# Kernel optimization log

Hardware: AMD Instinct MI355X
Metric: run time of the kernel (lower is better)

## Reference

```python
import jax, jax.numpy as jnp
import numpy as np

EPS = 1e-7
T_NCE = 0.07      # opt.nce_t
MOMENTUM = 0.5    # opt.nce_m
N_DATA = 100000   # opt.n_data


def l2norm(x):
    # Normalize(power=2): x / (sum(x^2, dim=1))^(1/2)
    return x / jnp.sqrt(jnp.sum(x * x, axis=1, keepdims=True))


def contrast_loss(x, P):
    # ContrastLoss (Eq 18). x: [B, P+K] of normalized exp-similarities.
    B, PK = x.shape
    N = PK - P
    m_pn = N * (1.0 / N_DATA)  # m * Pn
    pos = x[:, :P]                                   # [B, P]
    log_D1 = jnp.log(pos / (pos + m_pn + EPS))
    neg = x[:, P:]                                   # [B, N]
    log_D0 = jnp.log(m_pn / (neg + m_pn + EPS))
    # log_D0.view(-1,1).repeat(1,P).sum(0) == P copies of log_D0.sum()
    return -((log_D1.sum(0) + log_D0.sum()) / B).sum() / P


def setup_inputs() -> dict:
    key = jax.random.key(0)
    ks = jax.random.split(key, 10)
    B, S_DIM, T_DIM, FEAT = 64, 2048, 2048, 128
    P, K = 4, 8192
    NCLS, PER = 7, 1000
    stdv = 1.0 / np.sqrt(FEAT / 3.0)
    return {
        "f_s": jax.random.normal(ks[0], (B, S_DIM), jnp.float32),
        "f_t": jax.random.normal(ks[1], (B, T_DIM), jnp.float32),
        "idx": jax.random.randint(ks[2], (B,), 0, N_DATA),
        "batch_label": jax.random.uniform(ks[3], (B, NCLS), dtype=jnp.float32),
        "class_index": jax.random.randint(ks[4], (NCLS, PER), 0, N_DATA),
        "num_pos": P,
        "contrast_idx": jax.random.randint(ks[5], (B, P + K), 0, N_DATA),
        "W_s": jax.random.normal(ks[6], (S_DIM, FEAT), jnp.float32) * 0.02,
        "b_s": jnp.zeros((FEAT,), jnp.float32),
        "W_t": jax.random.normal(ks[7], (T_DIM, FEAT), jnp.float32) * 0.02,
        "b_t": jnp.zeros((FEAT,), jnp.float32),
        "memory_s": jax.random.uniform(ks[8], (N_DATA, FEAT), jnp.float32, -stdv, stdv),
        "memory_t": jax.random.uniform(ks[9], (N_DATA, FEAT), jnp.float32, -stdv, stdv),
    }


def reference(f_s, f_t, idx, batch_label, class_index, num_pos, contrast_idx,
              W_s, b_s, W_t, b_t, memory_s, memory_t):
    # Embed + L2 norm
    f_s = l2norm(f_s @ W_s + b_s)   # [B, D]
    f_t = l2norm(f_t @ W_t + b_t)   # [B, D]

    # ContrastMemory (memory banks are buffers -> no grad through them)
    mem_s = jax.lax.stop_gradient(memory_s)
    mem_t = jax.lax.stop_gradient(memory_t)

    w_t = mem_t[contrast_idx]                                     # [B, P+K, D]
    out_s = jnp.exp(jnp.einsum('bkd,bd->bk', w_t, f_s) / T_NCE)
    out_s = out_s / (jnp.mean(out_s) * N_DATA)                    # Z_s normalization
    w_s = mem_s[contrast_idx]                                     # [B, P+K, D]
    out_t = jnp.exp(jnp.einsum('bkd,bd->bk', w_s, f_t) / T_NCE)
    out_t = out_t / (jnp.mean(out_t) * N_DATA)                    # Z_t normalization

    # momentum memory update (done under no_grad in torch)
    upd_s = l2norm(mem_s[idx] * MOMENTUM + jax.lax.stop_gradient(f_s) * (1.0 - MOMENTUM))
    new_mem_s = mem_s.at[idx].set(upd_s)
    upd_t = l2norm(mem_t[idx] * MOMENTUM + jax.lax.stop_gradient(f_t) * (1.0 - MOMENTUM))
    new_mem_t = mem_t.at[idx].set(upd_t)

    CCD_loss = contrast_loss(out_s, num_pos) + contrast_loss(out_t, num_pos)

    # class-center anchors: gather per-class memory rows, relu, mean -> [NCLS, D]
    s_anchors = l2norm(jnp.mean(jax.nn.relu(new_mem_s[class_index]), axis=1))
    t_anchors = l2norm(jnp.mean(jax.nn.relu(new_mem_t[class_index]), axis=1))

    # anchor relation loss (anchors detached; teacher relation fully detached)
    s_rel = (f_s @ jax.lax.stop_gradient(s_anchors).T) / T_NCE    # [B, NCLS]
    t_rel = jax.lax.stop_gradient((f_t @ t_anchors.T) / T_NCE)
    targets = jax.nn.softmax(t_rel, axis=1)
    log_inputs = jax.nn.log_softmax(s_rel, axis=1)
    relation_loss = jnp.sum(targets * (jnp.log(targets + EPS * 0 + 1e-30) - log_inputs)) / s_rel.shape[0]

    return (CCD_loss, relation_loss, f_s, f_t)
```

## Files before the change

kernel.cpp:

```cpp
#include <hip/hip_runtime.h>
#include <math.h>
#include <stdint.h>

#define B 64
#define SDIM 2048
#define FEAT 128
#define P 4
#define PK 8196
#define NCLS 7
#define PER 1000
#define NDATA 100000
#define EPSC 1e-7f
#define M_PN 0.08192f
#define JCHUNKS 50
#define CS (PER / JCHUNKS)

#define DTSZ (64 * NDATA)
#define KSPLIT 4
#define KSEG 2049
#define KS1 8
#define TPW 4
#define ROWS_BLK (4 * TPW * 16)

#define TILE 16
#define WCHUNK 512
#define NT (WCHUNK / TILE)

#define GLL16(gp, lp) \
    __builtin_amdgcn_global_load_lds( \
        (__attribute__((address_space(1))) void*)(uintptr_t)(gp), \
        (__attribute__((address_space(3))) void*)(lp), 16, 0, 0)

typedef __attribute__((ext_vector_type(8))) short bf16x8;
typedef __attribute__((ext_vector_type(4))) float f32x4;

static __device__ __forceinline__ short f2bf(float x)
{
    union { float f; uint32_t u; } v; v.f = x;
    const uint32_t r = (v.u + 0x7fffu + ((v.u >> 16) & 1u)) >> 16;
    return (short)r;
}

__global__ void gemm_partial_kernel(const float* __restrict__ f_s,
                                    const float* __restrict__ f_t,
                                    const float* __restrict__ W_s,
                                    const float* __restrict__ W_t,
                                    float* __restrict__ fb)
{
    const int row = blockIdx.x;
    const int z   = blockIdx.y;
    const int ks  = blockIdx.z;
    const float* f = z == 0 ? f_s : f_t;
    const float* W = z == 0 ? W_s : W_t;

    const int t  = threadIdx.x;
    const int d  = t & 127;
    const int kh = t >> 7;

    __shared__ float frow[SDIM / KS1];
    frow[t] = f[row * SDIM + ks * (SDIM / KS1) + t];
    __syncthreads();

    float acc = 0.0f;
    const int kb = ks * (SDIM / KS1) + kh * 128;
    #pragma unroll 8
    for (int k = 0; k < 128; ++k)
        acc = fmaf(frow[kh * 128 + k], W[(kb + k) * FEAT + d], acc);

    __shared__ float part[2][128];
    part[kh][d] = acc;
    __syncthreads();
    if (t < 128)
        atomicAdd(&fb[((size_t)z * B + row) * FEAT + t], part[0][t] + part[1][t]);
}

__global__ void norm_finish_kernel(const float* __restrict__ fb,
                                   const float* __restrict__ b_s,
                                   const float* __restrict__ b_t,
                                   float* __restrict__ out_fs,
                                   float* __restrict__ out_ft,
                                   float* __restrict__ fsw,
                                   float* __restrict__ ftw,
                                   unsigned short* __restrict__ fsb,
                                   unsigned short* __restrict__ ftb)
{
    const int row = blockIdx.x;
    const int z   = blockIdx.y;
    const int d   = threadIdx.x;
    const float* bias = z == 0 ? b_s : b_t;
    float* out = z == 0 ? out_fs : out_ft;
    float* fw  = z == 0 ? fsw : ftw;
    unsigned short* fbx = z == 0 ? fsb : ftb;

    const float a = fb[((size_t)z * B + row) * FEAT + d] + bias[d];
    __shared__ float red[128];
    red[d] = a * a;
    __syncthreads();
    for (int s = 64; s > 0; s >>= 1) {
        if (d < s) red[d] += red[d + s];
        __syncthreads();
    }
    const float v = a * (1.0f / sqrtf(red[0]));
    out[row * FEAT + d] = v;
    fw[row * FEAT + d]  = v;
    fbx[row * FEAT + d] = (unsigned short)f2bf(v);
}

#define MFMA4(av, kc, a0, a1, a2, a3) do { \
    a0 = __builtin_amdgcn_mfma_f32_16x16x32_bf16(av, bv[kc][0], a0, 0, 0, 0); \
    a1 = __builtin_amdgcn_mfma_f32_16x16x32_bf16(av, bv[kc][1], a1, 0, 0, 0); \
    a2 = __builtin_amdgcn_mfma_f32_16x16x32_bf16(av, bv[kc][2], a2, 0, 0, 0); \
    a3 = __builtin_amdgcn_mfma_f32_16x16x32_bf16(av, bv[kc][3], a3, 0, 0, 0); \
    } while (0)

__global__ __launch_bounds__(256, 2)
void dgemm4_kernel(const unsigned short* __restrict__ fsb,
                   const unsigned short* __restrict__ ftb,
                   const float* __restrict__ mem_s,
                   const float* __restrict__ mem_t,
                   float* __restrict__ DT0,
                   float* __restrict__ DT1,
                   int zbase)
{
    const int z = blockIdx.y + zbase;
    const unsigned short* fWb = z == 0 ? fsb : ftb;
    const float* mem          = z == 0 ? mem_t : mem_s;
    float* DT                 = z == 0 ? DT0 : DT1;

    const int tid = threadIdx.x;
    const int w   = tid >> 6;
    const int l   = tid & 63;
    const int ln  = l & 15;
    const int ko  = l >> 4;
    const int xk  = ln & 7;
    const int wrowbase = blockIdx.x * ROWS_BLK + w * (TPW * 16);

    __shared__ __align__(16) float rows[4][2][16 * FEAT];

    bf16x8 bv[4][4];
    #pragma unroll
    for (int kc = 0; kc < 4; ++kc)
        #pragma unroll
        for (int nt = 0; nt < 4; ++nt)
            bv[kc][nt] = *(const bf16x8*)(fWb + (nt * 16 + ln) * FEAT + kc * 32 + ko * 8);

#define STG(tt, bf) do { \
    _Pragma("unroll") \
    for (int p_ = 0; p_ < 8; ++p_) { \
        const int r_ = 2 * p_ + (l >> 5); \
        int gr_ = wrowbase + (tt) * 16 + r_; \
        if (gr_ >= NDATA) gr_ = NDATA - 1; \
        const float* g_ = mem + (size_t)gr_ * FEAT + (((l & 31) ^ (r_ & 7)) << 2); \
        GLL16(g_, &rows[w][bf][p_ * 256]); \
    } } while (0)

    STG(0, 0);
    int cur = 0;
    for (int t = 0; t < TPW; ++t) {
        if (t + 1 < TPW) {
            STG(t + 1, cur ^ 1);
            asm volatile("s_waitcnt vmcnt(8)" ::: "memory");
        } else {
            asm volatile("s_waitcnt vmcnt(0)" ::: "memory");
        }
        __builtin_amdgcn_sched_barrier(0);

        const float* rb = &rows[w][cur][ln * FEAT];
        f32x4 c0 = (f32x4){0.f,0.f,0.f,0.f};
        f32x4 c1 = (f32x4){0.f,0.f,0.f,0.f};
        f32x4 c2 = (f32x4){0.f,0.f,0.f,0.f};
        f32x4 c3 = (f32x4){0.f,0.f,0.f,0.f};
        #pragma unroll
        for (int kc = 0; kc < 4; ++kc) {
            const int g0 = kc * 8 + ko * 2;
            const float4 lo = *(const float4*)(rb + (((g0 + 0) ^ xk) << 2));
            const float4 hi = *(const float4*)(rb + (((g0 + 1) ^ xk) << 2));
            const bf16x8 av = (bf16x8){ f2bf(lo.x), f2bf(lo.y), f2bf(lo.z), f2bf(lo.w),
                                        f2bf(hi.x), f2bf(hi.y), f2bf(hi.z), f2bf(hi.w) };
            MFMA4(av, kc, c0, c1, c2, c3);
        }

        const int growb = wrowbase + t * 16 + ko * 4;
        if (growb < NDATA) {
            *(f32x4*)(DT + (size_t)( 0 + ln) * NDATA + growb) = c0;
            *(f32x4*)(DT + (size_t)(16 + ln) * NDATA + growb) = c1;
            *(f32x4*)(DT + (size_t)(32 + ln) * NDATA + growb) = c2;
            *(f32x4*)(DT + (size_t)(48 + ln) * NDATA + growb) = c3;
        }
        cur ^= 1;
    }
#undef STG
}

__global__ void gather2_kernel(const int* __restrict__ contrast_idx,
                               const float* __restrict__ DT0,
                               const float* __restrict__ DT1,
                               float* __restrict__ out_raw,
                               float* __restrict__ Ssum)
{
    const int z   = blockIdx.z;
    const int b   = blockIdx.y;
    const int ks  = blockIdx.x;
    const int tid = threadIdx.x;
    const int k0  = ks * KSEG;
    const int kend = min(k0 + KSEG, PK);
    const float inv_t = 1.0f / 0.07f;
    const float* dtb = (z == 0 ? DT0 : DT1) + (size_t)b * NDATA;
    float* orz = out_raw + (size_t)z * (B * PK);
    float lsum = 0.0f;
    #pragma unroll 4
    for (int k = k0 + tid; k < kend; k += 256) {
        const int ci = contrast_idx[(size_t)b * PK + k];
        const float v = expf(dtb[ci] * inv_t);
        orz[(size_t)b * PK + k] = v;
        lsum += v;
    }
    __shared__ float red[256];
    red[tid] = lsum;
    __syncthreads();
    for (int s = 128; s > 0; s >>= 1) {
        if (tid < s) red[tid] += red[tid + s];
        __syncthreads();
    }
    if (tid == 0) atomicAdd(&Ssum[z], red[0]);
}

__global__ void gemm_norm_kernel(const float* __restrict__ f_s,
                                 const float* __restrict__ f_t,
                                 const float* __restrict__ W_s,
                                 const float* __restrict__ b_s,
                                 const float* __restrict__ W_t,
                                 const float* __restrict__ b_t,
                                 float* __restrict__ out_fs,
                                 float* __restrict__ out_ft)
{
    const int row = blockIdx.x;
    const int z   = blockIdx.y;
    const float* f    = z == 0 ? f_s : f_t;
    const float* W    = z == 0 ? W_s : W_t;
    const float* bias = z == 0 ? b_s : b_t;
    float* out        = z == 0 ? out_fs : out_ft;

    __shared__ __align__(16) float frow[SDIM];
    const int t  = threadIdx.x;
    const int d  = t & 127;
    const int kh = t >> 7;
    for (int k = t; k < SDIM; k += 256) frow[k] = f[row * SDIM + k];
    __syncthreads();

    float acc = 0.0f;
    const int k0 = kh * (SDIM / 2);
    for (int k = k0; k < k0 + SDIM / 2; ++k)
        acc = fmaf(frow[k], W[k * FEAT + d], acc);

    __shared__ float part[2][128];
    part[kh][d] = acc;
    __syncthreads();
    const float a = part[0][d] + part[1][d] + bias[d];

    __shared__ float red[256];
    red[t] = (t < 128) ? a * a : 0.0f;
    __syncthreads();
    for (int s = 128; s > 0; s >>= 1) {
        if (t < s) red[t] += red[t + s];
        __syncthreads();
    }
    if (t < 128) out[row * FEAT + t] = a * (1.0f / sqrtf(red[0]));
}

__global__ __launch_bounds__(64)
void dots_kernel(const float* __restrict__ fsn,
                 const float* __restrict__ ftn,
                 const int*   __restrict__ contrast_idx,
                 const float* __restrict__ mem_s,
                 const float* __restrict__ mem_t,
                 float* __restrict__ out_raw,
                 float* __restrict__ Ssum)
{
    const int z = blockIdx.z;
    const int b = blockIdx.y;
    const int l = threadIdx.x;
    const int kchunk = blockIdx.x * WCHUNK;

    const float* f   = (z == 0 ? fsn : ftn) + b * FEAT;
    const float* mem = (z == 0 ? mem_t : mem_s);

    __shared__ __align__(16) float rows[2][TILE * FEAT];
    __shared__ __align__(16) float fl[FEAT];
    __shared__ int cis[WCHUNK];

    fl[l]      = f[l];
    fl[l + 64] = f[l + 64];
    for (int i = l; i < WCHUNK; i += 64) {
        const int k = kchunk + i;
        cis[i] = contrast_idx[(size_t)b * PK + (k < PK ? k : PK - 1)];
    }
    __syncthreads();

    const int q   = l >> 4;
    const int r_c = l & 15;
    const int xk  = r_c & 7;
    const int rh  = l >> 5;
    const int sl  = l & 31;

    const float4* fg = (const float4*)fl;
    const float4 f0 = fg[q * 8 + 0], f1 = fg[q * 8 + 1];
    const float4 f2 = fg[q * 8 + 2], f3 = fg[q * 8 + 3];
    const float4 f4 = fg[q * 8 + 4], f5 = fg[q * 8 + 5];
    const float4 f6 = fg[q * 8 + 6], f7 = fg[q * 8 + 7];

    const float inv_t = 1.0f / 0.07f;
    const size_t obase = (size_t)z * (B * PK) + (size_t)b * PK;
    float lsum = 0.0f;

#define STAGE(tt, bf) do { \
    _Pragma("unroll") \
    for (int p_ = 0; p_ < 8; ++p_) { \
        const int rr_ = 2 * p_ + rh; \
        const int ci_ = cis[(tt) * TILE + rr_]; \
        const float* g_ = mem + (size_t)ci_ * FEAT + ((sl ^ (rr_ & 7)) << 2); \
        GLL16(g_, &rows[bf][p_ * 256]); \
    } } while (0)

    STAGE(0, 0);
    int cur = 0;
    for (int t = 0; t < NT; ++t) {
        if (t + 1 < NT) {
            STAGE(t + 1, cur ^ 1);
            asm volatile("s_waitcnt vmcnt(8)" ::: "memory");
        } else {
            asm volatile("s_waitcnt vmcnt(0)" ::: "memory");
        }
        __builtin_amdgcn_sched_barrier(0);

        const float* rbase = &rows[cur][r_c * FEAT];
        float dot;
        {
            const float4 m0 = *(const float4*)(rbase + (((q * 8 + 0) ^ xk) << 2));
            const float4 m1 = *(const float4*)(rbase + (((q * 8 + 1) ^ xk) << 2));
            const float4 m2 = *(const float4*)(rbase + (((q * 8 + 2) ^ xk) << 2));
            const float4 m3 = *(const float4*)(rbase + (((q * 8 + 3) ^ xk) << 2));
            const float4 m4 = *(const float4*)(rbase + (((q * 8 + 4) ^ xk) << 2));
            const float4 m5 = *(const float4*)(rbase + (((q * 8 + 5) ^ xk) << 2));
            const float4 m6 = *(const float4*)(rbase + (((q * 8 + 6) ^ xk) << 2));
            const float4 m7 = *(const float4*)(rbase + (((q * 8 + 7) ^ xk) << 2));
            dot = m0.x * f0.x;
            dot = fmaf(m0.y, f0.y, dot); dot = fmaf(m0.z, f0.z, dot); dot = fmaf(m0.w, f0.w, dot);
            dot = fmaf(m1.x, f1.x, dot); dot = fmaf(m1.y, f1.y, dot); dot = fmaf(m1.z, f1.z, dot); dot = fmaf(m1.w, f1.w, dot);
            dot = fmaf(m2.x, f2.x, dot); dot = fmaf(m2.y, f2.y, dot); dot = fmaf(m2.z, f2.z, dot); dot = fmaf(m2.w, f2.w, dot);
            dot = fmaf(m3.x, f3.x, dot); dot = fmaf(m3.y, f3.y, dot); dot = fmaf(m3.z, f3.z, dot); dot = fmaf(m3.w, f3.w, dot);
            dot = fmaf(m4.x, f4.x, dot); dot = fmaf(m4.y, f4.y, dot); dot = fmaf(m4.z, f4.z, dot); dot = fmaf(m4.w, f4.w, dot);
            dot = fmaf(m5.x, f5.x, dot); dot = fmaf(m5.y, f5.y, dot); dot = fmaf(m5.z, f5.z, dot); dot = fmaf(m5.w, f5.w, dot);
            dot = fmaf(m6.x, f6.x, dot); dot = fmaf(m6.y, f6.y, dot); dot = fmaf(m6.z, f6.z, dot); dot = fmaf(m6.w, f6.w, dot);
            dot = fmaf(m7.x, f7.x, dot); dot = fmaf(m7.y, f7.y, dot); dot = fmaf(m7.z, f7.z, dot); dot = fmaf(m7.w, f7.w, dot);
        }
        dot += __shfl_xor(dot, 16);
        dot += __shfl_xor(dot, 32);

        const int krow = kchunk + t * TILE + r_c;
        if (q == 0 && krow < PK) {
            const float val = expf(dot * inv_t);
            out_raw[obase + krow] = val;
            lsum += val;
        }
        cur ^= 1;
    }
#undef STAGE

    lsum += __shfl_xor(lsum, 8);
    lsum += __shfl_xor(lsum, 4);
    lsum += __shfl_xor(lsum, 2);
    lsum += __shfl_xor(lsum, 1);
    if (l == 0) atomicAdd(&Ssum[z], lsum);
}

__global__ void ccd_loss_kernel(const float* __restrict__ out_raw,
                                const float* __restrict__ Ssum,
                                float* __restrict__ acc)
{
    const int z = blockIdx.y;
    const float S = Ssum[z];
    const float c = ((float)(B * PK)) / (S * (float)NDATA);

    const int total = B * PK;
    float contrib = 0.0f;
    for (int i = blockIdx.x * blockDim.x + threadIdx.x; i < total;
         i += gridDim.x * blockDim.x) {
        const float v = out_raw[(size_t)z * total + i] * c;
        const int k = i % PK;
        if (k < P) {
            contrib += logf(v / (v + M_PN + EPSC));
        } else {
            contrib += (float)P * logf(M_PN / (v + M_PN + EPSC));
        }
    }
    __shared__ float red[256];
    red[threadIdx.x] = contrib;
    __syncthreads();
    for (int s = 128; s > 0; s >>= 1) {
        if (threadIdx.x < s) red[threadIdx.x] += red[threadIdx.x + s];
        __syncthreads();
    }
    if (threadIdx.x == 0) atomicAdd(&acc[z], red[0]);
}

__global__ void upd_kernel(const float* __restrict__ fsn,
                           const float* __restrict__ ftn,
                           const int*   __restrict__ idx,
                           const float* __restrict__ mem_s,
                           const float* __restrict__ mem_t,
                           float* __restrict__ upd)
{
    const int z = blockIdx.y;
    const int b = blockIdx.x;
    const int d = threadIdx.x;
    const float* mem = z == 0 ? mem_s : mem_t;
    const float* f   = z == 0 ? fsn : ftn;
    const int i = idx[b];
    const float v = mem[(size_t)i * FEAT + d] * 0.5f + f[b * FEAT + d] * 0.5f;
    __shared__ float red[128];
    red[d] = v * v;
    __syncthreads();
    for (int s = 64; s > 0; s >>= 1) {
        if (d < s) red[d] += red[d + s];
        __syncthreads();
    }
    upd[(size_t)z * (B * FEAT) + b * FEAT + d] = v * (1.0f / sqrtf(red[0]));
}

__global__ void remap_kernel(const int* __restrict__ class_index,
                             const int* __restrict__ idx,
                             int* __restrict__ remap)
{
    const int e = blockIdx.x * 256 + threadIdx.x;
    if (e >= NCLS * PER) return;
    const int ci = class_index[e];
    int rb = -1;
    for (int b = B - 1; b >= 0; --b) {
        if (idx[b] == ci) { rb = b; break; }
    }
    remap[e] = rb;
}

__global__ void anchors_partial_kernel(const int* __restrict__ class_index,
                                       const int* __restrict__ remap,
                                       const float* __restrict__ mem_s,
                                       const float* __restrict__ mem_t,
                                       const float* __restrict__ upd,
                                       float* __restrict__ partial)
{
    const int z     = blockIdx.z;
    const int c     = blockIdx.y;
    const int chunk = blockIdx.x;
    const int d     = threadIdx.x;
    const float* mem = z == 0 ? mem_s : mem_t;
    const float* u   = upd + (size_t)z * (B * FEAT);
    float acc = 0.0f;
    #pragma unroll 4
    for (int j = chunk * CS; j < chunk * CS + CS; ++j) {
        const int e = c * PER + j;
        const int ci = class_index[e];
        const int rb = remap[e];
        const float* row = (rb >= 0) ? (u + rb * FEAT) : (mem + (size_t)ci * FEAT);
        const float v = row[d];
        acc += v > 0.0f ? v : 0.0f;
    }
    atomicAdd(&partial[(size_t)z * (NCLS * FEAT) + c * FEAT + d], acc);
}

__global__ void anchors_finish_kernel(const float* __restrict__ partial,
                                      float* __restrict__ anchors)
{
    const int z = blockIdx.y;
    const int c = blockIdx.x;
    const int d = threadIdx.x;
    const float meanv = partial[(size_t)z * (NCLS * FEAT) + c * FEAT + d]
                        * (1.0f / (float)PER);
    __shared__ float red[128];
    red[d] = meanv * meanv;
    __syncthreads();
    for (int s = 64; s > 0; s >>= 1) {
        if (d < s) red[d] += red[d + s];
        __syncthreads();
    }
    anchors[(size_t)z * (NCLS * FEAT) + c * FEAT + d] = meanv * (1.0f / sqrtf(red[0]));
}

__global__ void final_kernel(const float* __restrict__ fsn,
                             const float* __restrict__ ftn,
                             const float* __restrict__ anchors,
                             const float* __restrict__ acc,
                             float* __restrict__ d_out)
{
    __shared__ float sa[NCLS * FEAT];
    __shared__ float ta[NCLS * FEAT];
    const int tid = threadIdx.x;
    for (int i = tid; i < NCLS * FEAT; i += 64) {
        sa[i] = anchors[i];
        ta[i] = anchors[NCLS * FEAT + i];
    }
    __syncthreads();

    const int b = tid;
    float srel[NCLS], trel[NCLS];
    for (int j = 0; j < NCLS; ++j) { srel[j] = 0.0f; trel[j] = 0.0f; }
    for (int d = 0; d < FEAT; ++d) {
        const float fs = fsn[b * FEAT + d];
        const float ft = ftn[b * FEAT + d];
        #pragma unroll
        for (int j = 0; j < NCLS; ++j) {
            srel[j] = fmaf(fs, sa[j * FEAT + d], srel[j]);
            trel[j] = fmaf(ft, ta[j * FEAT + d], trel[j]);
        }
    }
    const float inv_t = 1.0f / 0.07f;
    float smax = -1e30f, tmax = -1e30f;
    for (int j = 0; j < NCLS; ++j) {
        srel[j] *= inv_t; trel[j] *= inv_t;
        smax = fmaxf(smax, srel[j]);
        tmax = fmaxf(tmax, trel[j]);
    }
    float ssum = 0.0f, tsum = 0.0f;
    float texp[NCLS];
    for (int j = 0; j < NCLS; ++j) {
        ssum += expf(srel[j] - smax);
        texp[j] = expf(trel[j] - tmax);
        tsum += texp[j];
    }
    const float lse_s = logf(ssum);
    float contrib = 0.0f;
    for (int j = 0; j < NCLS; ++j) {
        const float tgt = texp[j] / tsum;
        const float log_in = srel[j] - smax - lse_s;
        contrib += tgt * (logf(tgt + 1e-30f) - log_in);
    }
    for (int off = 32; off > 0; off >>= 1) contrib += __shfl_down(contrib, off);
    if (tid == 0) {
        d_out[1] = contrib / (float)B;
        d_out[0] = -(acc[0] + acc[1]) / (float)(B * P);
    }
}

extern "C" void kernel_launch(void* const* d_in, const int* in_sizes, int n_in,
                              void* d_out_v, int out_size, void* d_ws, size_t ws_size,
                              hipStream_t stream)
{
    const float* f_s = (const float*)d_in[0];
    const float* f_t = (const float*)d_in[1];
    const int*   idx = (const int*)d_in[2];
    const int*   class_index = (const int*)d_in[4];
    const int*   contrast_idx = (const int*)d_in[6];
    const float* W_s = (const float*)d_in[7];
    const float* b_s = (const float*)d_in[8];
    const float* W_t = (const float*)d_in[9];
    const float* b_t = (const float*)d_in[10];
    const float* mem_s = (const float*)d_in[11];
    const float* mem_t = (const float*)d_in[12];

    float* out    = (float*)d_out_v;
    float* out_fs = out + 2;
    float* out_ft = out + 2 + B * FEAT;

    float* ws = (float*)d_ws;
    const size_t fl = ws_size / sizeof(float);
    const size_t REST = 2 * (size_t)B * PK
                      + 2 * B * FEAT
                      + 2 * (B * FEAT / 2)
                      + 2 * B * FEAT
                      + 2 * B * FEAT
                      + 4 * NCLS * FEAT
                      + NCLS * PER
                      + 64;
    const bool big   = fl >= 2 * (size_t)DTSZ + REST;
    const bool small = fl >= 1 * (size_t)DTSZ + REST;

    if (small) {
        float* DT0 = ws;
        float* DT1 = big ? ws + DTSZ : DT0;
        float* p   = (big ? ws + 2 * (size_t)DTSZ : ws + DTSZ);
        float* out_raw = p;            p += 2 * (size_t)B * PK;
        float* fsw     = p;            p += B * FEAT;
        float* ftw     = p;            p += B * FEAT;
        unsigned short* fsb = (unsigned short*)p;  p += B * FEAT / 2;
        unsigned short* ftb = (unsigned short*)p;  p += B * FEAT / 2;
        float* fb      = p;            p += 2 * B * FEAT;
        float* partial = p;            p += 2 * NCLS * FEAT;
        float* Ssum    = p;            p += 2;
        float* acc     = p;            p += 2;
        float* upd     = p;            p += 2 * B * FEAT;
        float* anchors = p;            p += 2 * NCLS * FEAT;
        int*   remap   = (int*)p;

        hipMemsetAsync(fb, 0,
                       (2 * B * FEAT + 2 * NCLS * FEAT + 4) * sizeof(float),
                       stream);

        dim3 g1a(B, 2, KS1);
        gemm_partial_kernel<<<g1a, 256, 0, stream>>>(f_s, f_t, W_s, W_t, fb);
        dim3 g1b(B, 2);
        norm_finish_kernel<<<g1b, 128, 0, stream>>>(fb, b_s, b_t,
                                                    out_fs, out_ft,
                                                    fsw, ftw, fsb, ftb);

        const int gblocks = (NDATA + ROWS_BLK - 1) / ROWS_BLK;
        if (big) {
            dim3 gd(gblocks, 2);
            dgemm4_kernel<<<gd, 256, 0, stream>>>(fsb, ftb, mem_s, mem_t,
                                                  DT0, DT1, 0);
            dim3 gg(KSPLIT, B, 2);
            gather2_kernel<<<gg, 256, 0, stream>>>(contrast_idx, DT0, DT1,
                                                   out_raw, Ssum);
        } else {
            dim3 gd(gblocks, 1);
            dim3 gg(KSPLIT, B, 1);
            dgemm4_kernel<<<gd, 256, 0, stream>>>(fsb, ftb, mem_s, mem_t,
                                                  DT0, DT0, 0);
            gather2_kernel<<<gg, 256, 0, stream>>>(contrast_idx, DT0, DT0,
                                                   out_raw, Ssum);
            dgemm4_kernel<<<gd, 256, 0, stream>>>(fsb, ftb, mem_s, mem_t,
                                                  DT0, DT0, 1);
            gather2_kernel<<<gg, 256, 0, stream>>>(contrast_idx, DT0, DT0,
                                                   out_raw + (size_t)B * PK,
                                                   Ssum + 1);
        }

        dim3 g3(256, 2);
        ccd_loss_kernel<<<g3, 256, 0, stream>>>(out_raw, Ssum, acc);
        dim3 g4(B, 2);
        upd_kernel<<<g4, 128, 0, stream>>>(out_fs, out_ft, idx, mem_s, mem_t, upd);
        remap_kernel<<<(NCLS * PER + 255) / 256, 256, 0, stream>>>(class_index, idx, remap);
        dim3 g5a(JCHUNKS, NCLS, 2);
        anchors_partial_kernel<<<g5a, 128, 0, stream>>>(class_index, remap,
                                                        mem_s, mem_t, upd, partial);
        dim3 g5b(NCLS, 2);
        anchors_finish_kernel<<<g5b, 128, 0, stream>>>(partial, anchors);
        final_kernel<<<1, 64, 0, stream>>>(out_fs, out_ft, anchors, acc, out);
    } else {
        float* out_raw = ws;
        float* upd     = out_raw + 2 * (B * PK);
        float* anchors = upd + 2 * (B * FEAT);
        float* partial = anchors + 2 * (NCLS * FEAT);
        float* Ssum    = partial + 2 * (NCLS * FEAT);
        float* acc     = Ssum + 2;
        int*   remap   = (int*)(acc + 2);

        hipMemsetAsync(partial, 0, (2 * NCLS * FEAT + 4) * sizeof(float), stream);

        dim3 g1(B, 2);
        gemm_norm_kernel<<<g1, 256, 0, stream>>>(f_s, f_t, W_s, b_s, W_t, b_t,
                                                 out_fs, out_ft);
        dim3 g2((PK + WCHUNK - 1) / WCHUNK, B, 2);
        dots_kernel<<<g2, 64, 0, stream>>>(out_fs, out_ft, contrast_idx,
                                           mem_s, mem_t, out_raw, Ssum);
        dim3 g3(256, 2);
        ccd_loss_kernel<<<g3, 256, 0, stream>>>(out_raw, Ssum, acc);
        dim3 g4(B, 2);
        upd_kernel<<<g4, 128, 0, stream>>>(out_fs, out_ft, idx, mem_s, mem_t, upd);
        remap_kernel<<<(NCLS * PER + 255) / 256, 256, 0, stream>>>(class_index, idx, remap);
        dim3 g5a(JCHUNKS, NCLS, 2);
        anchors_partial_kernel<<<g5a, 128, 0, stream>>>(class_index, remap,
                                                        mem_s, mem_t, upd, partial);
        dim3 g5b(NCLS, 2);
        anchors_finish_kernel<<<g5b, 128, 0, stream>>>(partial, anchors);
        final_kernel<<<1, 64, 0, stream>>>(out_fs, out_ft, anchors, acc, out);
    }
}
```

Baseline: 118.6 us.

## Recompute gathered similarities in a fused loss pass and shrink dgemm blocks

The gather kernel no longer writes the exponentiated similarities to a buffer. Instead it only accumulates the normalisation sum, and a second pass re-gathers from the dot-product table to compute the contrastive loss terms directly, which removes the separate ccd_loss kernel and the large out_raw round trip. The redundant fp32 copies of the normalised features are also dropped. The bf16 GEMM over the memory bank now uses 2 waves per block instead of 4, giving more, smaller blocks. The price is a second round of random gathers and exp evaluations over the dot-product table.

```diff
diff --git a/kernel.cpp b/kernel.cpp
--- a/kernel.cpp
+++ b/kernel.cpp
@@ -20,7 +20,8 @@
 #define KSEG 2049
 #define KS1 8
 #define TPW 4
-#define ROWS_BLK (4 * TPW * 16)
+#define WVS 2
+#define ROWS_BLK (WVS * TPW * 16)
 
 #define TILE 16
 #define WCHUNK 512
@@ -79,8 +80,6 @@
                                    const float* __restrict__ b_t,
                                    float* __restrict__ out_fs,
                                    float* __restrict__ out_ft,
-                                   float* __restrict__ fsw,
-                                   float* __restrict__ ftw,
                                    unsigned short* __restrict__ fsb,
                                    unsigned short* __restrict__ ftb)
 {
@@ -89,7 +88,6 @@
     const int d   = threadIdx.x;
     const float* bias = z == 0 ? b_s : b_t;
     float* out = z == 0 ? out_fs : out_ft;
-    float* fw  = z == 0 ? fsw : ftw;
     unsigned short* fbx = z == 0 ? fsb : ftb;
 
     const float a = fb[((size_t)z * B + row) * FEAT + d] + bias[d];
@@ -102,7 +100,6 @@
     }
     const float v = a * (1.0f / sqrtf(red[0]));
     out[row * FEAT + d] = v;
-    fw[row * FEAT + d]  = v;
     fbx[row * FEAT + d] = (unsigned short)f2bf(v);
 }
 
@@ -113,8 +110,8 @@
     a3 = __builtin_amdgcn_mfma_f32_16x16x32_bf16(av, bv[kc][3], a3, 0, 0, 0); \
     } while (0)
 
-__global__ __launch_bounds__(256, 2)
-void dgemm4_kernel(const unsigned short* __restrict__ fsb,
+__global__ __launch_bounds__(WVS * 64, 2)
+void dgemm5_kernel(const unsigned short* __restrict__ fsb,
                    const unsigned short* __restrict__ ftb,
                    const float* __restrict__ mem_s,
                    const float* __restrict__ mem_t,
@@ -135,7 +132,7 @@
     const int xk  = ln & 7;
     const int wrowbase = blockIdx.x * ROWS_BLK + w * (TPW * 16);
 
-    __shared__ __align__(16) float rows[4][2][16 * FEAT];
+    __shared__ __align__(16) float rows[WVS][2][16 * FEAT];
 
     bf16x8 bv[4][4];
     #pragma unroll
@@ -192,11 +189,10 @@
 #undef STG
 }
 
-__global__ void gather2_kernel(const int* __restrict__ contrast_idx,
-                               const float* __restrict__ DT0,
-                               const float* __restrict__ DT1,
-                               float* __restrict__ out_raw,
-                               float* __restrict__ Ssum)
+__global__ void gather_s_kernel(const int* __restrict__ contrast_idx,
+                                const float* __restrict__ DT0,
+                                const float* __restrict__ DT1,
+                                float* __restrict__ Ssum)
 {
     const int z   = blockIdx.z;
     const int b   = blockIdx.y;
@@ -206,14 +202,11 @@
     const int kend = min(k0 + KSEG, PK);
     const float inv_t = 1.0f / 0.07f;
     const float* dtb = (z == 0 ? DT0 : DT1) + (size_t)b * NDATA;
-    float* orz = out_raw + (size_t)z * (B * PK);
     float lsum = 0.0f;
     #pragma unroll 4
     for (int k = k0 + tid; k < kend; k += 256) {
         const int ci = contrast_idx[(size_t)b * PK + k];
-        const float v = expf(dtb[ci] * inv_t);
-        orz[(size_t)b * PK + k] = v;
-        lsum += v;
+        lsum += expf(dtb[ci] * inv_t);
     }
     __shared__ float red[256];
     red[tid] = lsum;
@@ -223,6 +216,40 @@
         __syncthreads();
     }
     if (tid == 0) atomicAdd(&Ssum[z], red[0]);
+}
+
+__global__ void loss2_kernel(const int* __restrict__ contrast_idx,
+                             const float* __restrict__ DT0,
+                             const float* __restrict__ DT1,
+                             const float* __restrict__ Ssum,
+                             float* __restrict__ acc)
+{
+    const int z   = blockIdx.z;
+    const int b   = blockIdx.y;
+    const int ks  = blockIdx.x;
+    const int tid = threadIdx.x;
+    const int k0  = ks * KSEG;
+    const int kend = min(k0 + KSEG, PK);
+    const float inv_t = 1.0f / 0.07f;
+    const float S = Ssum[z];
+    const float c = ((float)(B * PK)) / (S * (float)NDATA);
+    const float* dtb = (z == 0 ? DT0 : DT1) + (size_t)b * NDATA;
+    float contrib = 0.0f;
+    #pragma unroll 4
+    for (int k = k0 + tid; k < kend; k += 256) {
+        const int ci = contrast_idx[(size_t)b * PK + k];
+        const float v = expf(dtb[ci] * inv_t) * c;
+        if (k < P) contrib += logf(v / (v + M_PN + EPSC));
+        else       contrib += (float)P * logf(M_PN / (v + M_PN + EPSC));
+    }
+    __shared__ float red[256];
+    red[tid] = contrib;
+    __syncthreads();
+    for (int s = 128; s > 0; s >>= 1) {
+        if (tid < s) red[tid] += red[tid + s];
+        __syncthreads();
+    }
+    if (tid == 0) atomicAdd(&acc[z], red[0]);
 }
 
 __global__ void gemm_norm_kernel(const float* __restrict__ f_s,
@@ -563,9 +590,7 @@
 
     float* ws = (float*)d_ws;
     const size_t fl = ws_size / sizeof(float);
-    const size_t REST = 2 * (size_t)B * PK
-                      + 2 * B * FEAT
-                      + 2 * (B * FEAT / 2)
+    const size_t REST = (size_t)B * FEAT
                       + 2 * B * FEAT
                       + 2 * B * FEAT
                       + 4 * NCLS * FEAT
@@ -573,14 +598,12 @@
                       + 64;
     const bool big   = fl >= 2 * (size_t)DTSZ + REST;
     const bool small = fl >= 1 * (size_t)DTSZ + REST;
+    const size_t RESTFB = 2 * (size_t)B * PK + REST;
 
     if (small) {
         float* DT0 = ws;
         float* DT1 = big ? ws + DTSZ : DT0;
         float* p   = (big ? ws + 2 * (size_t)DTSZ : ws + DTSZ);
-        float* out_raw = p;            p += 2 * (size_t)B * PK;
-        float* fsw     = p;            p += B * FEAT;
-        float* ftw     = p;            p += B * FEAT;
         unsigned short* fsb = (unsigned short*)p;  p += B * FEAT / 2;
         unsigned short* ftb = (unsigned short*)p;  p += B * FEAT / 2;
         float* fb      = p;            p += 2 * B * FEAT;
@@ -599,33 +622,30 @@
         gemm_partial_kernel<<<g1a, 256, 0, stream>>>(f_s, f_t, W_s, W_t, fb);
         dim3 g1b(B, 2);
         norm_finish_kernel<<<g1b, 128, 0, stream>>>(fb, b_s, b_t,
-                                                    out_fs, out_ft,
-                                                    fsw, ftw, fsb, ftb);
+                                                    out_fs, out_ft, fsb, ftb);
 
         const int gblocks = (NDATA + ROWS_BLK - 1) / ROWS_BLK;
         if (big) {
             dim3 gd(gblocks, 2);
-            dgemm4_kernel<<<gd, 256, 0, stream>>>(fsb, ftb, mem_s, mem_t,
-                                                  DT0, DT1, 0);
+            dgemm5_kernel<<<gd, WVS * 64, 0, stream>>>(fsb, ftb, mem_s, mem_t,
+                                                       DT0, DT1, 0);
             dim3 gg(KSPLIT, B, 2);
-            gather2_kernel<<<gg, 256, 0, stream>>>(contrast_idx, DT0, DT1,
-                                                   out_raw, Ssum);
+            gather_s_kernel<<<gg, 256, 0, stream>>>(contrast_idx, DT0, DT1, Ssum);
+            loss2_kernel<<<gg, 256, 0, stream>>>(contrast_idx, DT0, DT1, Ssum, acc);
         } else {
             dim3 gd(gblocks, 1);
             dim3 gg(KSPLIT, B, 1);
-            dgemm4_kernel<<<gd, 256, 0, stream>>>(fsb, ftb, mem_s, mem_t,
-                                                  DT0, DT0, 0);
-            gather2_kernel<<<gg, 256, 0, stream>>>(contrast_idx, DT0, DT0,
-                                                   out_raw, Ssum);
-            dgemm4_kernel<<<gd, 256, 0, stream>>>(fsb, ftb, mem_s, mem_t,
-                                                  DT0, DT0, 1);
-            gather2_kernel<<<gg, 256, 0, stream>>>(contrast_idx, DT0, DT0,
-                                                   out_raw + (size_t)B * PK,
-                                                   Ssum + 1);
-        }
-
-        dim3 g3(256, 2);
-        ccd_loss_kernel<<<g3, 256, 0, stream>>>(out_raw, Ssum, acc);
+            dgemm5_kernel<<<gd, WVS * 64, 0, stream>>>(fsb, ftb, mem_s, mem_t,
+                                                       DT0, DT0, 0);
+            gather_s_kernel<<<gg, 256, 0, stream>>>(contrast_idx, DT0, DT0, Ssum);
+            loss2_kernel<<<gg, 256, 0, stream>>>(contrast_idx, DT0, DT0, Ssum, acc);
+            dgemm5_kernel<<<gd, WVS * 64, 0, stream>>>(fsb, ftb, mem_s, mem_t,
+                                                       DT0, DT0, 1);
+            gather_s_kernel<<<gg, 256, 0, stream>>>(contrast_idx, DT0, DT0, Ssum + 1);
+            loss2_kernel<<<gg, 256, 0, stream>>>(contrast_idx, DT0, DT0,
+                                                 Ssum + 1, acc + 1);
+        }
+
         dim3 g4(B, 2);
         upd_kernel<<<g4, 128, 0, stream>>>(out_fs, out_ft, idx, mem_s, mem_t, upd);
         remap_kernel<<<(NCLS * PER + 255) / 256, 256, 0, stream>>>(class_index, idx, remap);
@@ -636,6 +656,7 @@
         anchors_finish_kernel<<<g5b, 128, 0, stream>>>(partial, anchors);
         final_kernel<<<1, 64, 0, stream>>>(out_fs, out_ft, anchors, acc, out);
     } else {
+        (void)RESTFB;
         float* out_raw = ws;
         float* upd     = out_raw + 2 * (B * PK);
         float* anchors = upd + 2 * (B * FEAT);
```

Measured after the change: 129.5 us. +9.2%, slower.
